# Performance work log

Hardware: AMD Instinct MI355X
Metric: run time of the kernel (lower is better)

The kernel has to match this reference:

```python
import jax, jax.numpy as jnp
import numpy as np

N_NODES = 50000   # nodes per (single) node type
N_EDGES = 1000000 # edges per edge type (avg degree ~20)
IN_SIZE = 256
OUT_SIZE = 128
N_ETYPES = 3


def setup_inputs() -> dict:
    key = jax.random.key(0)
    k0, k1, k2, k3, k4 = jax.random.split(key, 5)
    x = jax.random.normal(k0, (N_NODES, IN_SIZE), jnp.float32)
    edge_src = jax.random.randint(k1, (N_ETYPES, N_EDGES), 0, N_NODES, jnp.int32)
    edge_dst = jax.random.randint(k2, (N_ETYPES, N_EDGES), 0, N_NODES, jnp.int32)
    # per-etype Linear params (weight stored as [in, out] so Wh = x @ W + b)
    W = jax.random.normal(k3, (N_ETYPES, IN_SIZE, OUT_SIZE), jnp.float32) / np.sqrt(IN_SIZE).astype(np.float32)
    b = jax.random.normal(k4, (N_ETYPES, OUT_SIZE), jnp.float32) * 0.01
    return {"x": x, "edge_src": edge_src, "edge_dst": edge_dst, "W": W, "b": b}


def reference(x, edge_src, edge_dst, W, b):
    # Per-etype linear projection: Wh[e] = x @ W[e] + b[e]  -> [E_types, N, OUT]
    Wh = jnp.einsum('ni,eio->eno', x, W) + b[:, None, :]

    def agg_one(wh, src, dst):
        # copy_u: gather projected src features along edges  [N_EDGES, OUT]
        msgs = wh[src]
        # mean reduce onto dst nodes (scatter-mean); zero for nodes w/o in-edges
        sums = jax.ops.segment_sum(msgs, dst, num_segments=N_NODES)
        deg = jax.ops.segment_sum(jnp.ones((N_EDGES,), wh.dtype), dst, num_segments=N_NODES)
        return jnp.where(deg[:, None] > 0, sums / jnp.maximum(deg, 1.0)[:, None], 0.0)

    h = jax.vmap(agg_one)(Wh, edge_src, edge_dst)  # [E_types, N, OUT]
    # agg='stack' cross-type reducer -> [N, E_types, OUT]
    return jnp.transpose(h, (1, 0, 2))
```

## Files before the change

### kernel.cpp

```cpp
#include <hip/hip_runtime.h>

#define N_NODES 50000
#define N_EDGES 1000000
#define N_ETYPES 3
#define NB 782
#define TOTB (N_ETYPES * NB)
#define EPB 8192
#define EPT 32
#define CAP 3072

typedef _Float16 f16x8 __attribute__((ext_vector_type(8)));
typedef float f32x4 __attribute__((ext_vector_type(4)));

__global__ void k_prep_w(const float* __restrict__ W, _Float16* __restrict__ Wt) {
    int e  = blockIdx.y;
    int id = blockIdx.x * blockDim.x + threadIdx.x;
    int k  = id >> 7;
    int n  = id & 127;
    Wt[(size_t)e * 32768 + (size_t)n * 256 + k] =
        (_Float16)W[(size_t)e * 32768 + (size_t)k * 128 + n];
}

__global__ void k_prep_x(const float* __restrict__ x, _Float16* __restrict__ x16) {
    int id = blockIdx.x * blockDim.x + threadIdx.x;
    const float* p = x + (size_t)id * 8;
    f32x4 lo = *(const f32x4*)p;
    f32x4 hi = *(const f32x4*)(p + 4);
    f16x8 v;
    #pragma unroll
    for (int j = 0; j < 4; ++j) {
        v[j]     = (_Float16)lo[j];
        v[j + 4] = (_Float16)hi[j];
    }
    *(f16x8*)(x16 + (size_t)id * 8) = v;
}

__global__ __launch_bounds__(256) void k_gemm(
    const _Float16* __restrict__ x16,
    const _Float16* __restrict__ Wt,
    const float* __restrict__ b,
    unsigned short* __restrict__ Wh)
{
    const int e    = blockIdx.y;
    const int tid  = threadIdx.x;
    const int lane = tid & 63;
    const int w    = tid >> 6;
    const int q    = lane >> 4;
    const int c    = lane & 15;
    const int rowBase = blockIdx.x * 128;
    const _Float16* Bt = Wt + (size_t)e * 32768;

    f32x4 acc[2][8];
    #pragma unroll
    for (int mt = 0; mt < 2; ++mt)
        #pragma unroll
        for (int nt = 0; nt < 8; ++nt)
            acc[mt][nt] = (f32x4){0.f, 0.f, 0.f, 0.f};

    int arow[2];
    #pragma unroll
    for (int mt = 0; mt < 2; ++mt) {
        int r = rowBase + w * 32 + mt * 16 + c;
        arow[mt] = (r < N_NODES) ? r : (N_NODES - 1);
    }

    #pragma unroll
    for (int ks = 0; ks < 8; ++ks) {
        f16x8 afrag[2];
        #pragma unroll
        for (int mt = 0; mt < 2; ++mt)
            afrag[mt] = *(const f16x8*)(x16 + (size_t)arow[mt] * 256 + ks * 32 + q * 8);
        #pragma unroll
        for (int nt = 0; nt < 8; ++nt) {
            f16x8 bfrag = *(const f16x8*)(Bt + (size_t)(nt * 16 + c) * 256 + ks * 32 + q * 8);
            #pragma unroll
            for (int mt = 0; mt < 2; ++mt)
                acc[mt][nt] = __builtin_amdgcn_mfma_f32_16x16x32_f16(
                    afrag[mt], bfrag, acc[mt][nt], 0, 0, 0);
        }
    }

    const size_t whBase = (size_t)e * N_NODES * 128;
    #pragma unroll
    for (int nt = 0; nt < 8; ++nt) {
        float bias = b[e * 128 + nt * 16 + c];
        #pragma unroll
        for (int mt = 0; mt < 2; ++mt) {
            int baseRow = rowBase + w * 32 + mt * 16 + q * 4;
            #pragma unroll
            for (int r = 0; r < 4; ++r) {
                int row = baseRow + r;
                if (row < N_NODES) {
                    float v = acc[mt][nt][r] + bias;
                    Wh[whBase + (size_t)row * 128 + nt * 16 + c] =
                        __builtin_bit_cast(unsigned short, (_Float16)v);
                }
            }
        }
    }
}

__global__ __launch_bounds__(256) void k_hist_b(const int* __restrict__ dst,
                                                int* __restrict__ cnt_b) {
    __shared__ int lcnt[NB];
    int e = blockIdx.y;
    for (int j = threadIdx.x; j < NB; j += 256) lcnt[j] = 0;
    __syncthreads();
    int beg = blockIdx.x * EPB;
    int end = beg + EPB; if (end > N_EDGES) end = N_EDGES;
    const int* de = dst + (size_t)e * N_EDGES;
    for (int i = beg + threadIdx.x; i < end; i += 256)
        atomicAdd(&lcnt[de[i] >> 6], 1);
    __syncthreads();
    for (int j = threadIdx.x; j < NB; j += 256) {
        int c = lcnt[j];
        if (c) atomicAdd(&cnt_b[e * NB + j], c);
    }
}

__global__ __launch_bounds__(1024) void k_scan(const int* __restrict__ cnt_b,
                                               int* __restrict__ offs_b,
                                               int* __restrict__ gcur) {
    int tid = threadIdx.x;
    int base = tid * 3;
    int v0 = (base     < TOTB) ? cnt_b[base]     : 0;
    int v1 = (base + 1 < TOTB) ? cnt_b[base + 1] : 0;
    int v2 = (base + 2 < TOTB) ? cnt_b[base + 2] : 0;
    int tsum = v0 + v1 + v2;
    int lane = tid & 63, wv = tid >> 6;
    int s = tsum;
    #pragma unroll
    for (int d = 1; d < 64; d <<= 1) {
        int t = __shfl_up(s, d);
        if (lane >= d) s += t;
    }
    __shared__ int wsum[16];
    __shared__ int woff[16];
    if (lane == 63) wsum[wv] = s;
    __syncthreads();
    if (tid == 0) {
        int a = 0;
        #pragma unroll
        for (int i = 0; i < 16; ++i) { int t = wsum[i]; woff[i] = a; a += t; }
    }
    __syncthreads();
    int texcl = s - tsum + woff[wv];
    if (base < TOTB)     { offs_b[base]     = texcl;           gcur[base]     = texcl; }
    if (base + 1 < TOTB) { offs_b[base + 1] = texcl + v0;      gcur[base + 1] = texcl + v0; }
    if (base + 2 < TOTB) { offs_b[base + 2] = texcl + v0 + v1; gcur[base + 2] = texcl + v0 + v1; }
}

__global__ __launch_bounds__(256) void k_fill_b(
    const int* __restrict__ src, const int* __restrict__ dst,
    int* __restrict__ gcur, unsigned* __restrict__ grec)
{
    __shared__ int lcnt[NB];
    __shared__ int lbase[NB];
    const int e   = blockIdx.y;
    const int tid = threadIdx.x;
    const int beg = blockIdx.x * EPB;
    const int* se = src + (size_t)e * N_EDGES;
    const int* de = dst + (size_t)e * N_EDGES;

    for (int j = tid; j < NB; j += 256) lcnt[j] = 0;
    __syncthreads();

    unsigned rec[EPT];
    int      bl [EPT];
    #pragma unroll
    for (int k = 0; k < EPT; ++k) {
        int i = beg + k * 256 + tid;
        if (i < N_EDGES) {
            int s = se[i];
            int d = de[i];
            int b = d >> 6;
            int lpos = atomicAdd(&lcnt[b], 1);
            rec[k] = (unsigned)s | ((unsigned)(d & 63) << 16);
            bl[k]  = b | (lpos << 10);
        } else {
            bl[k] = -1;
        }
    }
    __syncthreads();
    for (int j = tid; j < NB; j += 256) {
        int c = lcnt[j];
        lbase[j] = c ? atomicAdd(&gcur[e * NB + j], c) : 0;
    }
    __syncthreads();
    #pragma unroll
    for (int k = 0; k < EPT; ++k) {
        if (bl[k] >= 0) {
            int b    = bl[k] & 1023;
            int lpos = bl[k] >> 10;
            grec[lbase[b] + lpos] = rec[k];
        }
    }
}

__global__ __launch_bounds__(256) void k_bagg(
    const int* __restrict__ offs_b, const int* __restrict__ cnt_b,
    const unsigned* __restrict__ grec, const unsigned short* __restrict__ Wh,
    float* __restrict__ out)
{
    __shared__ unsigned       rec_s[CAP];
    __shared__ unsigned short nbr_s[CAP];
    __shared__ int ndeg[64], ncur[64], nstart[64];
    const int e    = blockIdx.y;
    const int bx   = blockIdx.x;
    const int tid  = threadIdx.x;
    const int lane = tid & 63;
    const int w    = tid >> 6;
    const int eb   = e * NB + bx;
    const int beg  = offs_b[eb];
    const int m    = cnt_b[eb];
    const unsigned* base = (const unsigned*)Wh + (size_t)e * N_NODES * 64;

    if (tid < 64) ndeg[tid] = 0;
    __syncthreads();

    if (m <= CAP) {
        for (int i = tid; i < m; i += 256) {
            unsigned r = grec[beg + i];
            rec_s[i] = r;
            atomicAdd(&ndeg[r >> 16], 1);
        }
        __syncthreads();
        if (tid < 64) {
            int v = ndeg[tid];
            int s = v;
            #pragma unroll
            for (int d = 1; d < 64; d <<= 1) {
                int t = __shfl_up(s, d);
                if (tid >= d) s += t;
            }
            int excl = s - v;
            nstart[tid] = excl;
            ncur[tid]   = excl;
        }
        __syncthreads();
        for (int i = tid; i < m; i += 256) {
            unsigned r = rec_s[i];
            int p = atomicAdd(&ncur[r >> 16], 1);
            nbr_s[p] = (unsigned short)(r & 0xFFFFu);
        }
        __syncthreads();

        for (int t = 0; t < 16; ++t) {
            int node = w * 16 + t;
            int st = nstart[node];
            int dg = ndeg[node];
            float a0 = 0.f, a1 = 0.f;
            for (int c0 = 0; c0 < dg; c0 += 64) {
                int mm = dg - c0; if (mm > 64) mm = 64;
                int idx = (c0 + lane < dg) ? (int)nbr_s[st + c0 + lane] : 0;
                int j = 0;
                for (; j + 8 <= mm; j += 8) {
                    unsigned u[8];
                    #pragma unroll
                    for (int k = 0; k < 8; ++k) {
                        int s = __builtin_amdgcn_readlane(idx, j + k);
                        u[k] = base[(size_t)s * 64 + lane];
                    }
                    #pragma unroll
                    for (int k = 0; k < 8; ++k) {
                        a0 += (float)__builtin_bit_cast(_Float16, (unsigned short)(u[k] & 0xFFFFu));
                        a1 += (float)__builtin_bit_cast(_Float16, (unsigned short)(u[k] >> 16));
                    }
                }
                if (j < mm) {
                    unsigned u[8];
                    #pragma unroll
                    for (int k = 0; k < 8; ++k) {
                        int jj = j + k;
                        int js = (jj < mm) ? jj : 0;
                        int s = __builtin_amdgcn_readlane(idx, js);
                        u[k] = base[(size_t)s * 64 + lane];
                    }
                    #pragma unroll
                    for (int k = 0; k < 8; ++k) {
                        if (j + k < mm) {
                            a0 += (float)__builtin_bit_cast(_Float16, (unsigned short)(u[k] & 0xFFFFu));
                            a1 += (float)__builtin_bit_cast(_Float16, (unsigned short)(u[k] >> 16));
                        }
                    }
                }
            }
            int n = bx * 64 + node;
            if (n < N_NODES) {
                float inv = (dg > 0) ? (1.0f / (float)dg) : 0.f;
                float2 o;
                o.x = a0 * inv;
                o.y = a1 * inv;
                *(float2*)(out + (size_t)n * 384 + e * 128 + 2 * lane) = o;
            }
        }
    } else {
        for (int i = tid; i < m; i += 256)
            atomicAdd(&ndeg[grec[beg + i] >> 16], 1);
        __syncthreads();
        for (int t = 0; t < 16; ++t) {
            int node = w * 16 + t;
            float a0 = 0.f, a1 = 0.f;
            for (int j0 = 0; j0 < m; j0 += 64) {
                int idx = (j0 + lane < m) ? (int)grec[beg + j0 + lane] : -1;
                int lim = m - j0; if (lim > 64) lim = 64;
                for (int k = 0; k < lim; ++k) {
                    int r = __builtin_amdgcn_readlane(idx, k);
                    if ((int)(((unsigned)r) >> 16) == node) {
                        unsigned u = base[(size_t)(r & 0xFFFFu) * 64 + lane];
                        a0 += (float)__builtin_bit_cast(_Float16, (unsigned short)(u & 0xFFFFu));
                        a1 += (float)__builtin_bit_cast(_Float16, (unsigned short)(u >> 16));
                    }
                }
            }
            int n = bx * 64 + node;
            if (n < N_NODES) {
                int dg = ndeg[node];
                float inv = (dg > 0) ? (1.0f / (float)dg) : 0.f;
                float2 o;
                o.x = a0 * inv;
                o.y = a1 * inv;
                *(float2*)(out + (size_t)n * 384 + e * 128 + 2 * lane) = o;
            }
        }
    }
}

extern "C" void kernel_launch(void* const* d_in, const int* in_sizes, int n_in,
                              void* d_out, int out_size, void* d_ws, size_t ws_size,
                              hipStream_t stream) {
    const float* x    = (const float*)d_in[0];
    const int*   esrc = (const int*)d_in[1];
    const int*   edst = (const int*)d_in[2];
    const float* W    = (const float*)d_in[3];
    const float* bias = (const float*)d_in[4];
    float*       out  = (float*)d_out;

    char* ws = (char*)d_ws;
    _Float16*       Wt  = (_Float16*)ws;
    _Float16*       x16 = (_Float16*)(ws + 196608);
    unsigned short* Wh  = (unsigned short*)(ws + 25796608);
    unsigned* grec = (unsigned*)(ws + 64196608);
    int* cnt_b     = (int*)(ws + 76196608);
    int* offs_b    = (int*)(ws + 76206080);
    int* gcur      = (int*)(ws + 76215552);

    hipMemsetAsync(cnt_b, 0, TOTB * sizeof(int), stream);

    k_prep_w<<<dim3(128, 3), 256, 0, stream>>>(W, Wt);
    k_prep_x<<<6250, 256, 0, stream>>>(x, x16);
    k_gemm<<<dim3(391, 3), 256, 0, stream>>>(x16, Wt, bias, Wh);

    const int FB = (N_EDGES + EPB - 1) / EPB;
    k_hist_b<<<dim3(FB, 3), 256, 0, stream>>>(edst, cnt_b);
    k_scan<<<1, 1024, 0, stream>>>(cnt_b, offs_b, gcur);
    k_fill_b<<<dim3(FB, 3), 256, 0, stream>>>(esrc, edst, gcur, grec);
    k_bagg<<<dim3(NB, 3), 256, 0, stream>>>(offs_b, cnt_b, grec, Wh, out);
}
```

Baseline: 393.7 us.

## Replace global atomic bucket cursors with per-block count scan; widen gather loads

The bucketing pipeline now writes each block's per-bucket histogram to a matrix, reduces it into bucket totals, and prefix-scans it per bucket. This gives k_fill_b deterministic write bases and removes the global atomics and the memset. Separately, the aggregation loop has each half-wave gather a different neighbor's row with 8-byte loads, then combines the halves with a cross-lane shuffle and writes float4. The cost is two extra small kernel launches plus some extra workspace traffic for the block-count matrix.

```diff
diff --git a/kernel.cpp b/kernel.cpp
--- a/kernel.cpp
+++ b/kernel.cpp
@@ -7,6 +7,8 @@
 #define TOTB (N_ETYPES * NB)
 #define EPB 8192
 #define EPT 32
+#define FB  ((N_EDGES + EPB - 1) / EPB)
+#define FBP 128
 #define CAP 3072
 
 typedef _Float16 f16x8 __attribute__((ext_vector_type(8)));
@@ -101,26 +103,36 @@
 }
 
 __global__ __launch_bounds__(256) void k_hist_b(const int* __restrict__ dst,
-                                                int* __restrict__ cnt_b) {
+                                                int* __restrict__ blkcnt) {
     __shared__ int lcnt[NB];
-    int e = blockIdx.y;
+    int e = blockIdx.y, blk = blockIdx.x;
     for (int j = threadIdx.x; j < NB; j += 256) lcnt[j] = 0;
     __syncthreads();
-    int beg = blockIdx.x * EPB;
+    int beg = blk * EPB;
     int end = beg + EPB; if (end > N_EDGES) end = N_EDGES;
     const int* de = dst + (size_t)e * N_EDGES;
     for (int i = beg + threadIdx.x; i < end; i += 256)
         atomicAdd(&lcnt[de[i] >> 6], 1);
     __syncthreads();
-    for (int j = threadIdx.x; j < NB; j += 256) {
-        int c = lcnt[j];
-        if (c) atomicAdd(&cnt_b[e * NB + j], c);
-    }
+    for (int j = threadIdx.x; j < NB; j += 256)
+        blkcnt[(size_t)(e * NB + j) * FBP + blk] = lcnt[j];
+}
+
+__global__ __launch_bounds__(256) void k_sumb(const int* __restrict__ blkcnt,
+                                              int* __restrict__ cnt_b) {
+    int lane = threadIdx.x & 63;
+    int wid = blockIdx.x * 4 + (threadIdx.x >> 6);
+    if (wid >= TOTB) return;
+    const int* p = blkcnt + (size_t)wid * FBP;
+    int v = 0;
+    for (int i = lane; i < FB; i += 64) v += p[i];
+    #pragma unroll
+    for (int d = 1; d < 64; d <<= 1) v += __shfl_xor(v, d);
+    if (lane == 0) cnt_b[wid] = v;
 }
 
 __global__ __launch_bounds__(1024) void k_scan(const int* __restrict__ cnt_b,
-                                               int* __restrict__ offs_b,
-                                               int* __restrict__ gcur) {
+                                               int* __restrict__ offs_b) {
     int tid = threadIdx.x;
     int base = tid * 3;
     int v0 = (base     < TOTB) ? cnt_b[base]     : 0;
@@ -145,20 +157,43 @@
     }
     __syncthreads();
     int texcl = s - tsum + woff[wv];
-    if (base < TOTB)     { offs_b[base]     = texcl;           gcur[base]     = texcl; }
-    if (base + 1 < TOTB) { offs_b[base + 1] = texcl + v0;      gcur[base + 1] = texcl + v0; }
-    if (base + 2 < TOTB) { offs_b[base + 2] = texcl + v0 + v1; gcur[base + 2] = texcl + v0 + v1; }
+    if (base < TOTB)     offs_b[base]     = texcl;
+    if (base + 1 < TOTB) offs_b[base + 1] = texcl + v0;
+    if (base + 2 < TOTB) offs_b[base + 2] = texcl + v0 + v1;
+}
+
+__global__ __launch_bounds__(256) void k_scan_blk(int* __restrict__ blkcnt,
+                                                  const int* __restrict__ offs_b) {
+    int lane = threadIdx.x & 63;
+    int wid = blockIdx.x * 4 + (threadIdx.x >> 6);
+    if (wid >= TOTB) return;
+    int* p = blkcnt + (size_t)wid * FBP;
+    int vA = p[lane];
+    int vB = (64 + lane < FB) ? p[64 + lane] : 0;
+    int sA = vA, sB = vB;
+    #pragma unroll
+    for (int d = 1; d < 64; d <<= 1) {
+        int t = __shfl_up(sA, d);
+        if (lane >= d) sA += t;
+        t = __shfl_up(sB, d);
+        if (lane >= d) sB += t;
+    }
+    int totA = __shfl(sA, 63);
+    int base = offs_b[wid];
+    p[lane] = base + sA - vA;
+    if (64 + lane < FB) p[64 + lane] = base + totA + sB - vB;
 }
 
 __global__ __launch_bounds__(256) void k_fill_b(
     const int* __restrict__ src, const int* __restrict__ dst,
-    int* __restrict__ gcur, unsigned* __restrict__ grec)
+    const int* __restrict__ blkcnt, unsigned* __restrict__ grec)
 {
     __shared__ int lcnt[NB];
     __shared__ int lbase[NB];
     const int e   = blockIdx.y;
+    const int blk = blockIdx.x;
     const int tid = threadIdx.x;
-    const int beg = blockIdx.x * EPB;
+    const int beg = blk * EPB;
     const int* se = src + (size_t)e * N_EDGES;
     const int* de = dst + (size_t)e * N_EDGES;
 
@@ -182,10 +217,8 @@
         }
     }
     __syncthreads();
-    for (int j = tid; j < NB; j += 256) {
-        int c = lcnt[j];
-        lbase[j] = c ? atomicAdd(&gcur[e * NB + j], c) : 0;
-    }
+    for (int j = tid; j < NB; j += 256)
+        lbase[j] = blkcnt[(size_t)(e * NB + j) * FBP + blk];
     __syncthreads();
     #pragma unroll
     for (int k = 0; k < EPT; ++k) {
@@ -210,6 +243,8 @@
     const int tid  = threadIdx.x;
     const int lane = tid & 63;
     const int w    = tid >> 6;
+    const int half = lane >> 5;
+    const int sub  = lane & 31;
     const int eb   = e * NB + bx;
     const int beg  = offs_b[eb];
     const int m    = cnt_b[eb];
@@ -249,49 +284,62 @@
             int node = w * 16 + t;
             int st = nstart[node];
             int dg = ndeg[node];
-            float a0 = 0.f, a1 = 0.f;
+            float a0 = 0.f, a1 = 0.f, a2 = 0.f, a3 = 0.f;
             for (int c0 = 0; c0 < dg; c0 += 64) {
                 int mm = dg - c0; if (mm > 64) mm = 64;
                 int idx = (c0 + lane < dg) ? (int)nbr_s[st + c0 + lane] : 0;
-                int j = 0;
-                for (; j + 8 <= mm; j += 8) {
-                    unsigned u[8];
+                int fullp = mm >> 1;
+                int p = 0;
+                for (; p + 8 <= fullp; p += 8) {
+                    uint2 u[8];
                     #pragma unroll
                     for (int k = 0; k < 8; ++k) {
-                        int s = __builtin_amdgcn_readlane(idx, j + k);
-                        u[k] = base[(size_t)s * 64 + lane];
+                        int r0 = 2 * (p + k);
+                        int s0 = __builtin_amdgcn_readlane(idx, r0);
+                        int s1 = __builtin_amdgcn_readlane(idx, r0 + 1);
+                        int s  = half ? s1 : s0;
+                        u[k] = *(const uint2*)(base + (size_t)s * 64 + (sub << 1));
                     }
                     #pragma unroll
                     for (int k = 0; k < 8; ++k) {
-                        a0 += (float)__builtin_bit_cast(_Float16, (unsigned short)(u[k] & 0xFFFFu));
-                        a1 += (float)__builtin_bit_cast(_Float16, (unsigned short)(u[k] >> 16));
+                        a0 += (float)__builtin_bit_cast(_Float16, (unsigned short)(u[k].x & 0xFFFFu));
+                        a1 += (float)__builtin_bit_cast(_Float16, (unsigned short)(u[k].x >> 16));
+                        a2 += (float)__builtin_bit_cast(_Float16, (unsigned short)(u[k].y & 0xFFFFu));
+                        a3 += (float)__builtin_bit_cast(_Float16, (unsigned short)(u[k].y >> 16));
                     }
                 }
-                if (j < mm) {
-                    unsigned u[8];
+                if (2 * p < mm) {
+                    uint2 u[8];
                     #pragma unroll
                     for (int k = 0; k < 8; ++k) {
-                        int jj = j + k;
-                        int js = (jj < mm) ? jj : 0;
-                        int s = __builtin_amdgcn_readlane(idx, js);
-                        u[k] = base[(size_t)s * 64 + lane];
+                        int r0 = 2 * (p + k);
+                        int r0c = (r0     < mm) ? r0     : 0;
+                        int r1c = (r0 + 1 < mm) ? r0 + 1 : 0;
+                        int s0 = __builtin_amdgcn_readlane(idx, r0c);
+                        int s1 = __builtin_amdgcn_readlane(idx, r1c);
+                        int s  = half ? s1 : s0;
+                        u[k] = *(const uint2*)(base + (size_t)s * 64 + (sub << 1));
                     }
                     #pragma unroll
                     for (int k = 0; k < 8; ++k) {
-                        if (j + k < mm) {
-                            a0 += (float)__builtin_bit_cast(_Float16, (unsigned short)(u[k] & 0xFFFFu));
-                            a1 += (float)__builtin_bit_cast(_Float16, (unsigned short)(u[k] >> 16));
+                        if (2 * (p + k) + half < mm) {
+                            a0 += (float)__builtin_bit_cast(_Float16, (unsigned short)(u[k].x & 0xFFFFu));
+                            a1 += (float)__builtin_bit_cast(_Float16, (unsigned short)(u[k].x >> 16));
+                            a2 += (float)__builtin_bit_cast(_Float16, (unsigned short)(u[k].y & 0xFFFFu));
+                            a3 += (float)__builtin_bit_cast(_Float16, (unsigned short)(u[k].y >> 16));
                         }
                     }
                 }
             }
+            a0 += __shfl_xor(a0, 32);
+            a1 += __shfl_xor(a1, 32);
+            a2 += __shfl_xor(a2, 32);
+            a3 += __shfl_xor(a3, 32);
             int n = bx * 64 + node;
-            if (n < N_NODES) {
+            if (half == 0 && n < N_NODES) {
                 float inv = (dg > 0) ? (1.0f / (float)dg) : 0.f;
-                float2 o;
-                o.x = a0 * inv;
-                o.y = a1 * inv;
-                *(float2*)(out + (size_t)n * 384 + e * 128 + 2 * lane) = o;
+                f32x4 o = {a0 * inv, a1 * inv, a2 * inv, a3 * inv};
+                *(f32x4*)(out + (size_t)n * 384 + e * 128 + (sub << 2)) = o;
             }
         }
     } else {
@@ -343,17 +391,16 @@
     unsigned* grec = (unsigned*)(ws + 64196608);
     int* cnt_b     = (int*)(ws + 76196608);
     int* offs_b    = (int*)(ws + 76206080);
-    int* gcur      = (int*)(ws + 76215552);
-
-    hipMemsetAsync(cnt_b, 0, TOTB * sizeof(int), stream);
+    int* blkcnt    = (int*)(ws + 76215552);
 
     k_prep_w<<<dim3(128, 3), 256, 0, stream>>>(W, Wt);
     k_prep_x<<<6250, 256, 0, stream>>>(x, x16);
     k_gemm<<<dim3(391, 3), 256, 0, stream>>>(x16, Wt, bias, Wh);
 
-    const int FB = (N_EDGES + EPB - 1) / EPB;
-    k_hist_b<<<dim3(FB, 3), 256, 0, stream>>>(edst, cnt_b);
-    k_scan<<<1, 1024, 0, stream>>>(cnt_b, offs_b, gcur);
-    k_fill_b<<<dim3(FB, 3), 256, 0, stream>>>(esrc, edst, gcur, grec);
+    k_hist_b<<<dim3(FB, 3), 256, 0, stream>>>(edst, blkcnt);
+    k_sumb<<<(TOTB + 3) / 4, 256, 0, stream>>>(blkcnt, cnt_b);
+    k_scan<<<1, 1024, 0, stream>>>(cnt_b, offs_b);
+    k_scan_blk<<<(TOTB + 3) / 4, 256, 0, stream>>>(blkcnt, offs_b);
+    k_fill_b<<<dim3(FB, 3), 256, 0, stream>>>(esrc, edst, blkcnt, grec);
     k_bagg<<<dim3(NB, 3), 256, 0, stream>>>(offs_b, cnt_b, grec, Wh, out);
 }
```

Result: faster. 383.1 us (-2.7%).
